# Optimization experiments

Measured on AMD Instinct MI355X. Metric: run time of the kernel, lower is better.

## Reference

```python
import jax, jax.numpy as jnp
import numpy as np

DIM = 1024
VOCAB = 32000
NSEQ = 32
LENGTHS = 64 - np.arange(NSEQ) // 2  # descending seq lengths 64..49 (packed seqs are length-sorted)


def setup_inputs() -> dict:
    key = jax.random.key(0)
    k1, k2, k3, k4, k5 = jax.random.split(key, 5)
    T = int(LENGTHS.max())
    batch_sizes = np.array([(LENGTHS > t).sum() for t in range(T)], dtype=np.int32)
    total = int(batch_sizes.sum())  # 1808 packed tokens
    hidden_states = jax.random.normal(k1, (total, 2 * DIM), dtype=jnp.float32)
    sentences = jax.random.randint(k2, (total,), 0, VOCAB, dtype=jnp.int32)
    weight = jax.random.normal(k3, (VOCAB, DIM), dtype=jnp.float32) * (1.0 / np.sqrt(DIM))
    fwd_bias = jax.random.normal(k4, (VOCAB,), dtype=jnp.float32) * 0.01
    bwd_bias = jax.random.normal(k5, (VOCAB,), dtype=jnp.float32) * 0.01
    return {
        "hidden_states": hidden_states,
        "weight": weight,
        "fwd_bias": fwd_bias,
        "bwd_bias": bwd_bias,
        "sentences": sentences,
        "batch_sizes": jnp.asarray(batch_sizes),
    }


def _build_indices(batch_sizes):
    # Static (host-side) index construction replicating the per-timestep Python loops.
    bs = np.asarray(batch_sizes)
    off = np.concatenate([[0], np.cumsum(bs)])  # start row of each timestep block
    T = len(bs)
    # forward: hidden at t-1 (first bs[t] rows) predicts token at t
    ctx_f = np.concatenate([off[t - 1] + np.arange(bs[t]) for t in range(1, T)])
    tgt_f = np.concatenate([off[t] + np.arange(bs[t]) for t in range(1, T)])
    # backward: hidden at i+1 predicts token at i (first bs[i+1] rows), i = T-2 .. 1
    ctx_b = np.concatenate([off[i + 1] + np.arange(bs[i + 1]) for i in range(1, T - 1)])
    tgt_b = np.concatenate([off[i] + np.arange(bs[i + 1]) for i in range(1, T - 1)])
    denom = float(2 * bs.sum() - bs[0] - bs[-1])
    return ctx_f, tgt_f, ctx_b, tgt_b, denom


def _ce_sum(h, W, b, tgt):
    # sum-reduced cross entropy: one fused GEMM over all packed rows
    logits = h @ W.T + b  # [N, V]
    lse = jax.nn.logsumexp(logits, axis=-1)  # [N]
    gold = jnp.take_along_axis(logits, tgt[:, None], axis=1)[:, 0]  # [N]
    return jnp.sum(lse - gold)


def reference(hidden_states, weight, fwd_bias, bwd_bias, sentences, batch_sizes):
    dim = hidden_states.shape[1] // 2
    ctx_f, tgt_f, ctx_b, tgt_b, denom = _build_indices(batch_sizes)
    loss_f = _ce_sum(hidden_states[ctx_f, :dim], weight, fwd_bias, sentences[tgt_f])
    loss_b = _ce_sum(hidden_states[ctx_b, dim:], weight, bwd_bias, sentences[tgt_b])
    return (loss_f + loss_b) / denom
```

## Files before the change

### kernel.cpp

```cpp
#include <hip/hip_runtime.h>
#include <hip/hip_bf16.h>
#include <stdint.h>

typedef float f32x4 __attribute__((ext_vector_type(4)));

#define LOG2E 1.4426950408889634f
#define WSCALE 16.0f
#define AS1 __attribute__((address_space(1)))
#define AS3 __attribute__((address_space(3)))


__device__ __forceinline__ uint32_t f32_to_e4m3(float x) {
    uint32_t ux = __float_as_uint(x);
    uint32_t s = (ux >> 24) & 0x80u;
    float a = __uint_as_float(ux & 0x7FFFFFFFu);
    if (a >= 448.0f) return s | 0x7Eu;
    int e = (int)((ux >> 23) & 0xFFu) - 127;
    if (e < -6) {
        int n = __float2int_rn(a * 512.0f);
        return s | (uint32_t)n;
    }
    uint32_t m = ux & 0x7FFFFFu;
    uint32_t r = (m + 0x7FFFFu + ((m >> 20) & 1u)) >> 20;
    if (r == 8u) { r = 0u; e += 1; }
    if (e > 8 || (e == 8 && r == 7u)) return s | 0x7Eu;
    return s | ((uint32_t)(e + 7) << 3) | r;
}

__device__ __forceinline__ uint2 cvt8_fp8(float4 v0, float4 v1, float sc) {
    uint32_t lo = f32_to_e4m3(v0.x * sc) | (f32_to_e4m3(v0.y * sc) << 8) |
                  (f32_to_e4m3(v0.z * sc) << 16) | (f32_to_e4m3(v0.w * sc) << 24);
    uint32_t hi = f32_to_e4m3(v1.x * sc) | (f32_to_e4m3(v1.y * sc) << 8) |
                  (f32_to_e4m3(v1.z * sc) << 16) | (f32_to_e4m3(v1.w * sc) << 24);
    return make_uint2(lo, hi);
}

__global__ void prep_kernel(const int* __restrict__ bs, int T,
                            const int* __restrict__ sentences,
                            int* __restrict__ hdr, float* __restrict__ fhdr,
                            int* __restrict__ row_ctx, int* __restrict__ row_tok) {
    __shared__ int off[1025];
    if (threadIdx.x == 0) {
        int acc = 0; off[0] = 0;
        for (int t = 0; t < T; ++t) { acc += bs[t]; off[t + 1] = acc; }
    }
    __syncthreads();
    const int total = off[T];
    const int Nf = total - off[1];
    const int Nb = total - off[2];
    for (int t = 1; t < T; ++t) {
        int start = off[t] - off[1];
        int cnt = off[t + 1] - off[t];
        for (int p = threadIdx.x; p < cnt; p += blockDim.x) {
            row_ctx[start + p] = off[t - 1] + p;
            row_tok[start + p] = sentences[off[t] + p];
        }
    }
    for (int i = 1; i < T - 1; ++i) {
        int start = Nf + off[i + 1] - off[2];
        int cnt = off[i + 2] - off[i + 1];
        for (int p = threadIdx.x; p < cnt; p += blockDim.x) {
            row_ctx[start + p] = off[i + 1] + p;
            row_tok[start + p] = sentences[off[i] + p];
        }
    }
    if (threadIdx.x == 0) {
        hdr[0] = Nf + Nb;
        hdr[1] = Nf;
        int bs0 = off[1];
        int bsl = off[T] - off[T - 1];
        fhdr[0] = (float)(2 * total - bs0 - bsl);
    }
}

__global__ void wconv_kernel(const float* __restrict__ W,
                             uint8_t* __restrict__ Wb, int K) {
    const int p = blockIdx.x >> 4, f = blockIdx.x & 15;
    char* panel = (char*)Wb + (size_t)p * ((size_t)K << 8);
    const int nch = 2 * K;
    for (int c = threadIdx.x; c < nch; c += 512) {
        const int t = c >> 6, l = c & 63;
        const int row = p * 256 + f * 16 + (l & 15);
        const int k = t * 32 + ((l >> 4) << 3);
        const float4* src = (const float4*)(W + (size_t)row * K + k);
        *(uint2*)(panel + (size_t)t * 8192 + f * 512 + l * 8) = cvt8_fp8(src[0], src[1], WSCALE);
    }
}

__global__ void gather_kernel(const float* __restrict__ hs,
                              const int* __restrict__ row_ctx,
                              const int* __restrict__ hdr,
                              uint8_t* __restrict__ Hc,
                              float* __restrict__ S, int D2, int K) {
    const int p = blockIdx.x >> 3, f = blockIdx.x & 7;
    const int M = hdr[0], Nf = hdr[1];
    if (f == 0 && threadIdx.x < 128) S[p * 128 + threadIdx.x] = 0.f;
    char* panel = (char*)Hc + (size_t)p * ((size_t)K << 7);
    const int nch = 2 * K;
    for (int c = threadIdx.x; c < nch; c += 512) {
        const int t = c >> 6, l = c & 63;
        const int row = p * 128 + f * 16 + (l & 15);
        char* d = panel + (size_t)t * 4096 + f * 512 + l * 8;
        if (row >= M) {
            *(uint2*)d = make_uint2(0u, 0u);
        } else {
            const int ctx = row_ctx[row];
            const int k = t * 32 + ((l >> 4) << 3);
            const float4* src = (const float4*)(hs + (size_t)ctx * D2 + (row < Nf ? 0 : K) + k);
            *(uint2*)d = cvt8_fp8(src[0], src[1], 1.0f);
        }
    }
}

__global__ __launch_bounds__(512, 4)
void gemm_lse(const uint8_t* __restrict__ A,
              const uint8_t* __restrict__ B,
              const float* __restrict__ fb,
              const float* __restrict__ bb,
              float* __restrict__ S,
              const int* __restrict__ hdr, int K, int MT) {
    const int M = hdr[0], Nf = hdr[1];

    const int nwg = gridDim.x, orig = blockIdx.x;
    const int q = nwg >> 3, rr = nwg & 7;
    const int xcd = orig & 7, i8 = orig >> 3;
    const int wgid = (xcd < rr ? xcd * (q + 1) : rr * (q + 1) + (xcd - rr) * q) + i8;
    const int bm = wgid % MT, bn = wgid / MT;
    if (bm * 128 >= M) return;

    __shared__ __align__(16) char lA[2][8192];
    __shared__ __align__(16) char lB[2][16384];

    const int tid = threadIdx.x, lane = tid & 63, wid = tid >> 6;
    const int wm = wid >> 2, wn = wid & 3;

    f32x4 acc[4][4];
#pragma unroll
    for (int i = 0; i < 4; ++i)
#pragma unroll
        for (int j = 0; j < 4; ++j) acc[i][j] = (f32x4)0.f;

    const char* Ap = (const char*)A + (size_t)bm * ((size_t)K << 7);
    const char* Bp = (const char*)B + (size_t)bn * ((size_t)K << 8);
    const int sd = tid << 4;
    const int ao = ((wm * 4) << 9) + (lane << 3);
    const int bo = ((wn * 4) << 9) + (lane << 3);

#define GLDS(src, dst) __builtin_amdgcn_global_load_lds(                      \
        (const AS1 uint32_t*)(src), (AS3 uint32_t*)(dst), 16, 0, 0)

#define STAGE(buf, s) do {                                                    \
    GLDS(Ap + ((size_t)(s) << 13) + sd,        lA[buf] + sd);                 \
    GLDS(Bp + ((size_t)(s) << 14) + sd,        lB[buf] + sd);                 \
    GLDS(Bp + ((size_t)(s) << 14) + 8192 + sd, lB[buf] + 8192 + sd);          \
} while (0)

#define COMPUTE(buf) do {                                                     \
    long a[8], b[8];                                                          \
    _Pragma("unroll")                                                         \
    for (int kk = 0; kk < 2; ++kk) {                                          \
        _Pragma("unroll")                                                     \
        for (int mf = 0; mf < 4; ++mf)                                        \
            a[kk * 4 + mf] = *(const long*)(lA[buf] + kk * 4096 + ao + (mf << 9)); \
        _Pragma("unroll")                                                     \
        for (int nf = 0; nf < 4; ++nf)                                        \
            b[kk * 4 + nf] = *(const long*)(lB[buf] + kk * 8192 + bo + (nf << 9)); \
    }                                                                         \
    __builtin_amdgcn_s_setprio(1);                                            \
    _Pragma("unroll")                                                         \
    for (int kk = 0; kk < 2; ++kk)                                            \
        _Pragma("unroll")                                                     \
        for (int mf = 0; mf < 4; ++mf)                                        \
            _Pragma("unroll")                                                 \
            for (int nf = 0; nf < 4; ++nf)                                    \
                acc[mf][nf] = __builtin_amdgcn_mfma_f32_16x16x32_fp8_fp8(     \
                    a[kk * 4 + mf], b[kk * 4 + nf], acc[mf][nf], 0, 0, 0);    \
    __builtin_amdgcn_s_setprio(0);                                            \
} while (0)

#define BAR() do { __builtin_amdgcn_s_barrier(); __builtin_amdgcn_sched_barrier(0); } while (0)

    const int NT = K >> 6;

    STAGE(0, 0);
    for (int t = 0; t < NT - 1; ++t) {
        STAGE((t + 1) & 1, t + 1);
        asm volatile("s_waitcnt vmcnt(3)" ::: "memory");
        BAR();
        COMPUTE(t & 1);
        BAR();
    }
    asm volatile("s_waitcnt vmcnt(0)" ::: "memory");
    BAR();
    COMPUTE((NT - 1) & 1);

    float fbv[4], bbv[4];
#pragma unroll
    for (int nf = 0; nf < 4; ++nf) {
        const int v = bn * 256 + wn * 64 + nf * 16 + (lane & 15);
        fbv[nf] = fb[v] * LOG2E; bbv[nf] = bb[v] * LOG2E;
    }
    const float k1 = LOG2E / WSCALE;
#pragma unroll
    for (int mf = 0; mf < 4; ++mf) {
#pragma unroll
        for (int j = 0; j < 4; ++j) {
            const int m = bm * 128 + wm * 64 + mf * 16 + ((lane >> 4) << 2) + j;
            if (m >= M) continue;
            const bool isf = m < Nf;
            float ps = 0.f;
#pragma unroll
            for (int nf = 0; nf < 4; ++nf)
                ps += exp2f(fmaf(acc[mf][nf][j], k1, isf ? fbv[nf] : bbv[nf]));
#pragma unroll
            for (int s = 1; s < 16; s <<= 1) ps += __shfl_xor(ps, s);
            if ((lane & 15) == 0) atomicAdd(&S[m], ps);
        }
    }
#undef GLDS
#undef STAGE
#undef COMPUTE
#undef BAR
}

__global__ void lse_naive(const float* __restrict__ hs,
                          const float* __restrict__ W,
                          const float* __restrict__ fb,
                          const float* __restrict__ bb,
                          const int* __restrict__ row_ctx,
                          const int* __restrict__ hdr,
                          float* __restrict__ S, int D2, int D, int V) {
    const int m = blockIdx.x;
    const int M = hdr[0], Nf = hdr[1];
    if (m >= M) return;
    __shared__ float hrow[2048];
    const int ctx = row_ctx[m];
    const float* h = hs + (size_t)ctx * D2 + (m < Nf ? 0 : D);
    for (int i = threadIdx.x; i < D; i += blockDim.x) hrow[i] = h[i];
    __syncthreads();
    const float* bias = (m < Nf) ? fb : bb;
    float ps = 0.f;
    for (int v = threadIdx.x; v < V; v += blockDim.x) {
        const float* w = W + (size_t)v * D;
        float dot = 0.f;
        for (int k = 0; k < D; ++k) dot = fmaf(hrow[k], w[k], dot);
        ps += exp2f((dot + bias[v]) * LOG2E);
    }
#pragma unroll
    for (int d = 1; d < 64; d <<= 1) ps += __shfl_xor(ps, d);
    __shared__ float wsum[4];
    const int wid = threadIdx.x >> 6, lane = threadIdx.x & 63;
    if (lane == 0) wsum[wid] = ps;
    __syncthreads();
    if (threadIdx.x == 0) S[m] = wsum[0] + wsum[1] + wsum[2] + wsum[3];
}

__global__ void gold_kernel(const float* __restrict__ hs,
                            const float* __restrict__ W,
                            const float* __restrict__ fb,
                            const float* __restrict__ bb,
                            const int* __restrict__ row_ctx,
                            const int* __restrict__ row_tok,
                            const int* __restrict__ hdr,
                            float* __restrict__ goldv, int D2, int D) {
    const int m = blockIdx.x;
    const int M = hdr[0];
    if (m >= M) return;
    const int Nf = hdr[1];
    const int ctx = row_ctx[m], tok = row_tok[m];
    const float4* h = (const float4*)(hs + (size_t)ctx * D2 + (m < Nf ? 0 : D));
    const float4* w = (const float4*)(W + (size_t)tok * D);
    float s = 0.f;
    for (int i = threadIdx.x; i < D / 4; i += blockDim.x) {
        float4 a = h[i], b = w[i];
        s += a.x * b.x + a.y * b.y + a.z * b.z + a.w * b.w;
    }
#pragma unroll
    for (int d = 1; d < 64; d <<= 1) s += __shfl_xor(s, d);
    __shared__ float wsum[4];
    const int wid = threadIdx.x >> 6, lane = threadIdx.x & 63;
    if (lane == 0) wsum[wid] = s;
    __syncthreads();
    if (threadIdx.x == 0) {
        float tot = wsum[0] + wsum[1] + wsum[2] + wsum[3];
        tot += (m < Nf ? fb[tok] : bb[tok]);
        goldv[m] = tot;
    }
}

__global__ void final_kernel(const float* __restrict__ S,
                             const float* __restrict__ goldv,
                             const int* __restrict__ hdr,
                             const float* __restrict__ fhdr,
                             float* __restrict__ out) {
    const int M = hdr[0];
    float s = 0.f;
    for (int m = threadIdx.x; m < M; m += blockDim.x)
        s += logf(S[m]) - goldv[m];
#pragma unroll
    for (int d = 1; d < 64; d <<= 1) s += __shfl_xor(s, d);
    __shared__ float wsum[4];
    const int wid = threadIdx.x >> 6, lane = threadIdx.x & 63;
    if (lane == 0) wsum[wid] = s;
    __syncthreads();
    if (threadIdx.x == 0)
        out[0] = (wsum[0] + wsum[1] + wsum[2] + wsum[3]) / fhdr[0];
}

extern "C" void kernel_launch(void* const* d_in, const int* in_sizes, int n_in,
                              void* d_out, int out_size, void* d_ws, size_t ws_size,
                              hipStream_t stream) {
    const float* hs  = (const float*)d_in[0];
    const float* W   = (const float*)d_in[1];
    const float* fb  = (const float*)d_in[2];
    const float* bb  = (const float*)d_in[3];
    const int* sent  = (const int*)d_in[4];
    const int* bs    = (const int*)d_in[5];
    const int total  = in_sizes[4];
    const int T      = in_sizes[5];
    const int V      = in_sizes[2];
    const int D      = in_sizes[1] / V;
    const int D2     = in_sizes[0] / total;
    const int Mcap   = ((2 * total) + 127) & ~127;
    const int MT     = Mcap / 128;
    const int NN     = V / 256;

    char* p = (char*)d_ws;
    int*   hdr     = (int*)p;            p += 256;
    float* fhdr    = (float*)p;          p += 256;
    int*   row_ctx = (int*)p;            p += (size_t)Mcap * 4;
    int*   row_tok = (int*)p;            p += (size_t)Mcap * 4;
    float* S       = (float*)p;          p += (size_t)Mcap * 4;
    float* goldv   = (float*)p;          p += (size_t)Mcap * 4;
    uint8_t* Hc    = (uint8_t*)p;        p += (size_t)Mcap * D;
    uint8_t* Wb    = (uint8_t*)p;
    const size_t need_wb = (size_t)(p - (char*)d_ws) + (size_t)V * D;

    prep_kernel<<<1, 256, 0, stream>>>(bs, T, sent, hdr, fhdr, row_ctx, row_tok);

    if (ws_size >= need_wb) {
        gather_kernel<<<MT * 8, 512, 0, stream>>>(hs, row_ctx, hdr, Hc, S, D2, D);
        wconv_kernel<<<(V / 256) * 16, 512, 0, stream>>>(W, Wb, D);
        gemm_lse<<<NN * MT, 512, 0, stream>>>(Hc, Wb, fb, bb, S, hdr, D, MT);
    } else {
        lse_naive<<<Mcap, 256, 0, stream>>>(hs, W, fb, bb, row_ctx, hdr, S, D2, D, V);
    }

    gold_kernel<<<Mcap, 256, 0, stream>>>(hs, W, fb, bb, row_ctx, row_tok, hdr, goldv, D2, D);
    final_kernel<<<1, 256, 0, stream>>>(S, goldv, hdr, fhdr, (float*)d_out);
}
```

Measured before the change: 278.9 us.

## Switch FP8 GEMM to 32x32x64 scaled MFMA with matching operand layout

Replaces the 16x16x32 fp8 MFMA inner loop with the gfx950 32x32x64 f8f6f4 scaled MFMA, using four 32x32 accumulators per wave instead of sixteen 16x16 tiles. The packed A and W fp8 layouts in gather and wconv are rewritten to 16-byte fragments that match the new instruction's operand pattern, and the LSE epilogue is adapted to the 32x32 accumulator layout. This is meant to cut MFMA issue count and LDS read instructions per K step, in exchange for changed conversion kernels and a wider shuffle reduction in the epilogue.

```diff
diff --git a/kernel.cpp b/kernel.cpp
--- a/kernel.cpp
+++ b/kernel.cpp
@@ -2,7 +2,9 @@
 #include <hip/hip_bf16.h>
 #include <stdint.h>
 
-typedef float f32x4 __attribute__((ext_vector_type(4)));
+typedef float f32x16 __attribute__((ext_vector_type(16)));
+typedef int   i32x4  __attribute__((ext_vector_type(4)));
+typedef int   i32x8  __attribute__((ext_vector_type(8)));
 
 #define LOG2E 1.4426950408889634f
 #define WSCALE 16.0f
@@ -27,12 +29,16 @@
     return s | ((uint32_t)(e + 7) << 3) | r;
 }
 
-__device__ __forceinline__ uint2 cvt8_fp8(float4 v0, float4 v1, float sc) {
-    uint32_t lo = f32_to_e4m3(v0.x * sc) | (f32_to_e4m3(v0.y * sc) << 8) |
-                  (f32_to_e4m3(v0.z * sc) << 16) | (f32_to_e4m3(v0.w * sc) << 24);
-    uint32_t hi = f32_to_e4m3(v1.x * sc) | (f32_to_e4m3(v1.y * sc) << 8) |
-                  (f32_to_e4m3(v1.z * sc) << 16) | (f32_to_e4m3(v1.w * sc) << 24);
-    return make_uint2(lo, hi);
+__device__ __forceinline__ uint32_t pack4_fp8(const float* s, float sc) {
+    return f32_to_e4m3(s[0] * sc) | (f32_to_e4m3(s[1] * sc) << 8) |
+           (f32_to_e4m3(s[2] * sc) << 16) | (f32_to_e4m3(s[3] * sc) << 24);
+}
+
+__device__ __forceinline__ uint4 cvt16_fp8(const float* s, float sc) {
+    uint4 r;
+    r.x = pack4_fp8(s, sc);      r.y = pack4_fp8(s + 4, sc);
+    r.z = pack4_fp8(s + 8, sc);  r.w = pack4_fp8(s + 12, sc);
+    return r;
 }
 
 __global__ void prep_kernel(const int* __restrict__ bs, int T,
@@ -75,15 +81,16 @@
 
 __global__ void wconv_kernel(const float* __restrict__ W,
                              uint8_t* __restrict__ Wb, int K) {
-    const int p = blockIdx.x >> 4, f = blockIdx.x & 15;
+    const int p = blockIdx.x >> 3, f = blockIdx.x & 7;
     char* panel = (char*)Wb + (size_t)p * ((size_t)K << 8);
-    const int nch = 2 * K;
+    const int row0 = p * 256 + f * 32;
+    const int nch = (K >> 6) << 7;
     for (int c = threadIdx.x; c < nch; c += 512) {
-        const int t = c >> 6, l = c & 63;
-        const int row = p * 256 + f * 16 + (l & 15);
-        const int k = t * 32 + ((l >> 4) << 3);
-        const float4* src = (const float4*)(W + (size_t)row * K + k);
-        *(uint2*)(panel + (size_t)t * 8192 + f * 512 + l * 8) = cvt8_fp8(src[0], src[1], WSCALE);
+        const int t = c >> 7, h = (c >> 6) & 1, l = c & 63;
+        const int row = row0 + (l & 31);
+        const int k = t * 64 + ((l >> 5) << 5) + h * 16;
+        *(uint4*)(panel + (size_t)t * 16384 + f * 2048 + h * 1024 + l * 16) =
+            cvt16_fp8(W + (size_t)row * K + k, WSCALE);
     }
 }
 
@@ -92,24 +99,34 @@
                               const int* __restrict__ hdr,
                               uint8_t* __restrict__ Hc,
                               float* __restrict__ S, int D2, int K) {
-    const int p = blockIdx.x >> 3, f = blockIdx.x & 7;
+    const int p = blockIdx.x >> 2, f = blockIdx.x & 3;
     const int M = hdr[0], Nf = hdr[1];
     if (f == 0 && threadIdx.x < 128) S[p * 128 + threadIdx.x] = 0.f;
     char* panel = (char*)Hc + (size_t)p * ((size_t)K << 7);
-    const int nch = 2 * K;
+    const int row0 = p * 128 + f * 32;
+    const int nch = (K >> 6) << 7;
     for (int c = threadIdx.x; c < nch; c += 512) {
-        const int t = c >> 6, l = c & 63;
-        const int row = p * 128 + f * 16 + (l & 15);
-        char* d = panel + (size_t)t * 4096 + f * 512 + l * 8;
+        const int t = c >> 7, h = (c >> 6) & 1, l = c & 63;
+        const int row = row0 + (l & 31);
+        char* d = panel + (size_t)t * 8192 + f * 2048 + h * 1024 + l * 16;
         if (row >= M) {
-            *(uint2*)d = make_uint2(0u, 0u);
+            uint4 z; z.x = z.y = z.z = z.w = 0u;
+            *(uint4*)d = z;
         } else {
             const int ctx = row_ctx[row];
-            const int k = t * 32 + ((l >> 4) << 3);
-            const float4* src = (const float4*)(hs + (size_t)ctx * D2 + (row < Nf ? 0 : K) + k);
-            *(uint2*)d = cvt8_fp8(src[0], src[1], 1.0f);
+            const int k = t * 64 + ((l >> 5) << 5) + h * 16;
+            *(uint4*)d = cvt16_fp8(hs + (size_t)ctx * D2 + (row < Nf ? 0 : K) + k, 1.0f);
         }
     }
+}
+
+__device__ __forceinline__ i32x8 ld_frag(const char* base) {
+    i32x4 lo = *(const i32x4*)(base);
+    i32x4 hi = *(const i32x4*)(base + 1024);
+    i32x8 r;
+    r[0] = lo[0]; r[1] = lo[1]; r[2] = lo[2]; r[3] = lo[3];
+    r[4] = hi[0]; r[5] = hi[1]; r[6] = hi[2]; r[7] = hi[3];
+    return r;
 }
 
 __global__ __launch_bounds__(512, 4)
@@ -134,17 +151,14 @@
     const int tid = threadIdx.x, lane = tid & 63, wid = tid >> 6;
     const int wm = wid >> 2, wn = wid & 3;
 
-    f32x4 acc[4][4];
-#pragma unroll
-    for (int i = 0; i < 4; ++i)
-#pragma unroll
-        for (int j = 0; j < 4; ++j) acc[i][j] = (f32x4)0.f;
+    f32x16 acc00 = (f32x16)0.f, acc01 = (f32x16)0.f;
+    f32x16 acc10 = (f32x16)0.f, acc11 = (f32x16)0.f;
 
     const char* Ap = (const char*)A + (size_t)bm * ((size_t)K << 7);
     const char* Bp = (const char*)B + (size_t)bn * ((size_t)K << 8);
     const int sd = tid << 4;
-    const int ao = ((wm * 4) << 9) + (lane << 3);
-    const int bo = ((wn * 4) << 9) + (lane << 3);
+    const int ao = ((wm * 2) << 11) + (lane << 4);
+    const int bo = ((wn * 2) << 11) + (lane << 4);
 
 #define GLDS(src, dst) __builtin_amdgcn_global_load_lds(                      \
         (const AS1 uint32_t*)(src), (AS3 uint32_t*)(dst), 16, 0, 0)
@@ -156,25 +170,19 @@
 } while (0)
 
 #define COMPUTE(buf) do {                                                     \
-    long a[8], b[8];                                                          \
-    _Pragma("unroll")                                                         \
-    for (int kk = 0; kk < 2; ++kk) {                                          \
-        _Pragma("unroll")                                                     \
-        for (int mf = 0; mf < 4; ++mf)                                        \
-            a[kk * 4 + mf] = *(const long*)(lA[buf] + kk * 4096 + ao + (mf << 9)); \
-        _Pragma("unroll")                                                     \
-        for (int nf = 0; nf < 4; ++nf)                                        \
-            b[kk * 4 + nf] = *(const long*)(lB[buf] + kk * 8192 + bo + (nf << 9)); \
-    }                                                                         \
+    i32x8 a0 = ld_frag(lA[buf] + ao);                                         \
+    i32x8 a1 = ld_frag(lA[buf] + ao + 2048);                                  \
+    i32x8 b0 = ld_frag(lB[buf] + bo);                                         \
+    i32x8 b1 = ld_frag(lB[buf] + bo + 2048);                                  \
     __builtin_amdgcn_s_setprio(1);                                            \
-    _Pragma("unroll")                                                         \
-    for (int kk = 0; kk < 2; ++kk)                                            \
-        _Pragma("unroll")                                                     \
-        for (int mf = 0; mf < 4; ++mf)                                        \
-            _Pragma("unroll")                                                 \
-            for (int nf = 0; nf < 4; ++nf)                                    \
-                acc[mf][nf] = __builtin_amdgcn_mfma_f32_16x16x32_fp8_fp8(     \
-                    a[kk * 4 + mf], b[kk * 4 + nf], acc[mf][nf], 0, 0, 0);    \
+    acc00 = __builtin_amdgcn_mfma_scale_f32_32x32x64_f8f6f4(                  \
+        a0, b0, acc00, 0, 0, 0, 127, 0, 127);                                 \
+    acc01 = __builtin_amdgcn_mfma_scale_f32_32x32x64_f8f6f4(                  \
+        a0, b1, acc01, 0, 0, 0, 127, 0, 127);                                 \
+    acc10 = __builtin_amdgcn_mfma_scale_f32_32x32x64_f8f6f4(                  \
+        a1, b0, acc10, 0, 0, 0, 127, 0, 127);                                 \
+    acc11 = __builtin_amdgcn_mfma_scale_f32_32x32x64_f8f6f4(                  \
+        a1, b1, acc11, 0, 0, 0, 127, 0, 127);                                 \
     __builtin_amdgcn_s_setprio(0);                                            \
 } while (0)
 
@@ -194,33 +202,35 @@
     BAR();
     COMPUTE((NT - 1) & 1);
 
-    float fbv[4], bbv[4];
-#pragma unroll
-    for (int nf = 0; nf < 4; ++nf) {
-        const int v = bn * 256 + wn * 64 + nf * 16 + (lane & 15);
-        fbv[nf] = fb[v] * LOG2E; bbv[nf] = bb[v] * LOG2E;
-    }
     const float k1 = LOG2E / WSCALE;
-#pragma unroll
-    for (int mf = 0; mf < 4; ++mf) {
-#pragma unroll
-        for (int j = 0; j < 4; ++j) {
-            const int m = bm * 128 + wm * 64 + mf * 16 + ((lane >> 4) << 2) + j;
-            if (m >= M) continue;
-            const bool isf = m < Nf;
-            float ps = 0.f;
-#pragma unroll
-            for (int nf = 0; nf < 4; ++nf)
-                ps += exp2f(fmaf(acc[mf][nf][j], k1, isf ? fbv[nf] : bbv[nf]));
-#pragma unroll
-            for (int s = 1; s < 16; s <<= 1) ps += __shfl_xor(ps, s);
-            if ((lane & 15) == 0) atomicAdd(&S[m], ps);
-        }
-    }
+    const int v0 = bn * 256 + wn * 64 + (lane & 31);
+    const float fbv0 = fb[v0] * LOG2E,      bbv0 = bb[v0] * LOG2E;
+    const float fbv1 = fb[v0 + 32] * LOG2E, bbv1 = bb[v0 + 32] * LOG2E;
+    const int mb0 = bm * 128 + wm * 64 + ((lane >> 5) << 2);
+
+#define EPI(T0, T1, MB) do {                                                  \
+    _Pragma("unroll")                                                         \
+    for (int reg = 0; reg < 16; ++reg) {                                      \
+        const int m = (MB) + (reg & 3) + ((reg >> 2) << 3);                   \
+        if (m < M) {            \
+            const bool isf = m < Nf;                                          \
+            float ps = exp2f(fmaf(T0[reg], k1, isf ? fbv0 : bbv0))            \
+                     + exp2f(fmaf(T1[reg], k1, isf ? fbv1 : bbv1));           \
+            _Pragma("unroll")                                                 \
+            for (int s = 1; s < 32; s <<= 1) ps += __shfl_xor(ps, s);         \
+            if ((lane & 31) == 0) atomicAdd(&S[m], ps);                       \
+        }                                                                     \
+    }                                                                         \
+} while (0)
+
+    EPI(acc00, acc01, mb0);
+    EPI(acc10, acc11, mb0 + 32);
+
 #undef GLDS
 #undef STAGE
 #undef COMPUTE
 #undef BAR
+#undef EPI
 }
 
 __global__ void lse_naive(const float* __restrict__ hs,
@@ -339,8 +349,8 @@
     prep_kernel<<<1, 256, 0, stream>>>(bs, T, sent, hdr, fhdr, row_ctx, row_tok);
 
     if (ws_size >= need_wb) {
-        gather_kernel<<<MT * 8, 512, 0, stream>>>(hs, row_ctx, hdr, Hc, S, D2, D);
-        wconv_kernel<<<(V / 256) * 16, 512, 0, stream>>>(W, Wb, D);
+        gather_kernel<<<MT * 4, 512, 0, stream>>>(hs, row_ctx, hdr, Hc, S, D2, D);
+        wconv_kernel<<<(V / 256) * 8, 512, 0, stream>>>(W, Wb, D);
         gemm_lse<<<NN * MT, 512, 0, stream>>>(Hc, Wb, fb, bb, S, hdr, D, MT);
     } else {
         lse_naive<<<Mcap, 256, 0, stream>>>(hs, W, fb, bb, row_ctx, hdr, S, D2, D, V);
```

After: 441.4 us. 1.58x slower.
